# Performance work log

Measured on AMD Instinct MI355X. Metric: run time of the kernel, lower is better.

Reference implementation:

```python
import jax, jax.numpy as jnp
import numpy as np

B, C, H, W = 4, 64, 64, 64

def _conv1x1(x, w, b):
    # Conv2d(k=1): y[b,o,h,w] = sum_c x[b,c,h,w]*w[o,c] + b[o]
    return jnp.einsum('bchw,oc->bohw', x, w) + b[None, :, None, None]

def setup_inputs() -> dict:
    key = jax.random.key(0)
    ks = jax.random.split(key, 8)
    s = 1.0 / np.sqrt(C)
    return {
        'v1': jax.random.normal(ks[0], (B, C, H, W), jnp.float32),
        'v2': jax.random.normal(ks[1], (B, C, H, W), jnp.float32),
        'wq': jax.random.normal(ks[2], (C, C), jnp.float32) * s,
        'bq': jax.random.normal(ks[3], (C,), jnp.float32) * 0.01,
        'wk': jax.random.normal(ks[4], (C, C), jnp.float32) * s,
        'bk': jax.random.normal(ks[5], (C,), jnp.float32) * 0.01,
        'wv': jax.random.normal(ks[6], (C, C), jnp.float32) * s,
        'bv': jax.random.normal(ks[7], (C,), jnp.float32) * 0.01,
    }

def reference(v1, v2, wq, bq, wk, bk, wv, bv):
    q = _conv1x1(v1, wq, bq)   # (B,C,H,W)
    k = _conv1x1(v2, wk, bk)
    v = _conv1x1(v2, wv, bv)
    b, c, h, w = q.shape
    n = c * h                   # tokens = C*H, feature dim = W (matches torch view)
    qf = q.reshape(b, n, w)
    kf = k.reshape(b, n, w)
    vf = v.reshape(b, n, w)
    scores = jnp.einsum('bnw,bmw->bnm', qf, kf)   # (B, N, N)
    attn = jax.nn.softmax(scores, axis=-1)
    out = jnp.einsum('bnm,bmw->bnw', attn, vf)
    return out.reshape(v1.shape)
```

## Files before the change

### kernel.cpp

```cpp
#include <hip/hip_runtime.h>


#define Bn 4
#define Cc 64
#define HW 4096
#define Nn 4096
#define Dd 64
#define TS (Bn * Nn * Dd)
#define LOG2E 1.44269504088896340736f

typedef _Float16 f16;
typedef _Float16 f16x8 __attribute__((ext_vector_type(8)));
typedef _Float16 f16x4 __attribute__((ext_vector_type(4)));
typedef __fp16 fp16x2 __attribute__((ext_vector_type(2)));
typedef float f32x4 __attribute__((ext_vector_type(4)));

__device__ __forceinline__ int swz(int row, int col) {
    return row * 64 + (col ^ ((row & 7) << 3));
}

__device__ __forceinline__ void gl_lds16(const f16* g, f16* l) {
    __builtin_amdgcn_global_load_lds(
        (const __attribute__((address_space(1))) unsigned int*)g,
        (__attribute__((address_space(3))) unsigned int*)l, 16, 0, 0);
}

__global__ __launch_bounds__(256) void qkv_conv(
    const float* __restrict__ v1, const float* __restrict__ v2,
    const float* __restrict__ wq, const float* __restrict__ bq,
    const float* __restrict__ wk, const float* __restrict__ bk,
    const float* __restrict__ wv, const float* __restrict__ bv,
    f16* __restrict__ Qh, f16* __restrict__ Kh, f16* __restrict__ Vh)
{
    const int t    = threadIdx.x;
    const int lane = t & 63;
    const int og   = __builtin_amdgcn_readfirstlane(t >> 6);
    const int b    = blockIdx.y;
    const int p    = blockIdx.x * 64 + lane;
    const int z    = blockIdx.z;
    const int zt   = z >> 1;
    const int ch0  = (z & 1) * 32 + og * 8;

    const float* w    = (zt == 0) ? wq : (zt == 1) ? wk : wv;
    const float* bias = (zt == 0) ? bq : (zt == 1) ? bk : bv;
    const float* x    = ((zt == 0) ? v1 : v2) + (size_t)b * (Cc * HW) + p;

    float acc[8];
    #pragma unroll
    for (int j = 0; j < 8; ++j) acc[j] = bias[ch0 + j];
    #pragma unroll 16
    for (int c = 0; c < 64; ++c) {
        float xc = x[c * HW];
        #pragma unroll
        for (int j = 0; j < 8; ++j)
            acc[j] = fmaf(w[(ch0 + j) * 64 + c], xc, acc[j]);
    }

    f16* dst = (zt == 0) ? Qh : (zt == 1) ? Kh : Vh;
    const float scale = (zt == 0) ? LOG2E : 1.0f;
    #pragma unroll
    for (int j = 0; j < 8; ++j) {
        size_t idx = (size_t)b * (Nn * Dd) + (size_t)(ch0 + j) * 4096 + p;
        dst[idx] = (f16)(acc[j] * scale);
    }
}

__global__ __launch_bounds__(256) void vtrans(const f16* __restrict__ Vh,
                                              f16* __restrict__ Vt)
{
    __shared__ f16 tile[64][72];
    const int t  = threadIdx.x;
    const int n0 = blockIdx.x * 64;
    const int b  = blockIdx.y;
    for (int i = t; i < 4096; i += 256) {
        int r = i >> 6, c = i & 63;
        tile[r][c] = Vh[(size_t)b * (Nn * Dd) + (size_t)(n0 + r) * 64 + c];
    }
    __syncthreads();
    for (int i = t; i < 4096; i += 256) {
        int w = i >> 6, n = i & 63;
        Vt[(size_t)b * (Dd * Nn) + (size_t)w * Nn + n0 + n] = tile[n][w];
    }
}

__global__ __launch_bounds__(512, 4) void attn(
    const f16* __restrict__ Qhg, const f16* __restrict__ Khg,
    const f16* __restrict__ Vtg,
    float* __restrict__ out, f16* __restrict__ Opart, float* __restrict__ lw)
{
    __shared__ __align__(16) f16 KT[2][4096];
    __shared__ __align__(16) f16 VT[2][4096];

    const int t    = threadIdx.x;
    const int lane = t & 63, wvi = t >> 6;
    const int g = lane >> 4, c = lane & 15;
    const int b  = blockIdx.z;
    const int sp = blockIdx.y;
    const int S  = gridDim.y;
    const int n0 = blockIdx.x * 256;
    const int keysPerSplit = Nn / S;
    const int nTiles = keysPerSplit / 64;
    const int kbase = sp * keysPerSplit;

    const int srow = t >> 3;
    const int gc   = ((t & 7) ^ (srow & 7)) * 8;
    f16* ldsKdst0 = &KT[0][(wvi * 8) * 64];
    f16* ldsKdst1 = &KT[1][(wvi * 8) * 64];
    f16* ldsVdst0 = &VT[0][(wvi * 8) * 64];
    f16* ldsVdst1 = &VT[1][(wvi * 8) * 64];

    const f16* Kb = Khg + (size_t)b * (Nn * Dd);
    const f16* Vb = Vtg + (size_t)b * (Dd * Nn);

    f16x8 qbh[2][2];
    #pragma unroll
    for (int qf = 0; qf < 2; ++qf) {
        const int qrow = n0 + wvi * 32 + qf * 16 + c;
        const f16* qhp = Qhg + ((size_t)b * Nn + qrow) * 64;
        #pragma unroll
        for (int ks = 0; ks < 2; ++ks)
            qbh[qf][ks] = *(const f16x8*)(qhp + ks * 32 + g * 8);
    }

    float m_run[2] = {-1e30f, -1e30f}, lpart[2] = {0.f, 0.f};
    f32x4 of[2][4];
    #pragma unroll
    for (int qf = 0; qf < 2; ++qf)
        #pragma unroll
        for (int nf = 0; nf < 4; ++nf)
            #pragma unroll
            for (int r = 0; r < 4; ++r) of[qf][nf][r] = 0.f;

    gl_lds16(Kb + (size_t)(kbase + srow) * 64 + gc, ldsKdst0);
    gl_lds16(Vb + (size_t)srow * Nn + kbase + gc, ldsVdst0);
    __syncthreads();
    int cur = 0;

    for (int kt = 0; kt < nTiles; ++kt) {
        if (kt + 1 < nTiles) {
            const int k0n = kbase + (kt + 1) * 64;
            f16* kd = cur ? ldsKdst0 : ldsKdst1;
            f16* vd = cur ? ldsVdst0 : ldsVdst1;
            gl_lds16(Kb + (size_t)(k0n + srow) * 64 + gc, kd);
            gl_lds16(Vb + (size_t)srow * Nn + k0n + gc, vd);
        }

        const f16* KTc = KT[cur];
        const f16* VTc = VT[cur];

        f32x4 accS[2][4];
        #pragma unroll
        for (int qf = 0; qf < 2; ++qf)
            #pragma unroll
            for (int fm = 0; fm < 4; ++fm)
                #pragma unroll
                for (int r = 0; r < 4; ++r) accS[qf][fm][r] = 0.f;
        #pragma unroll
        for (int fm = 0; fm < 4; ++fm) {
            const int key = fm * 16 + c;
            f16x8 kh0 = *(const f16x8*)(KTc + swz(key, g * 8));
            f16x8 kh1 = *(const f16x8*)(KTc + swz(key, 32 + g * 8));
            #pragma unroll
            for (int qf = 0; qf < 2; ++qf) {
                accS[qf][fm] = __builtin_amdgcn_mfma_f32_16x16x32_f16(kh0, qbh[qf][0], accS[qf][fm], 0, 0, 0);
                accS[qf][fm] = __builtin_amdgcn_mfma_f32_16x16x32_f16(kh1, qbh[qf][1], accS[qf][fm], 0, 0, 0);
            }
        }

        f16x4 pb[2][4];
        #pragma unroll
        for (int qf = 0; qf < 2; ++qf) {
            float m0 = fmaxf(fmaxf(accS[qf][0][0], accS[qf][0][1]),
                             fmaxf(accS[qf][0][2], accS[qf][0][3]));
            float m1 = fmaxf(fmaxf(accS[qf][1][0], accS[qf][1][1]),
                             fmaxf(accS[qf][1][2], accS[qf][1][3]));
            float m2 = fmaxf(fmaxf(accS[qf][2][0], accS[qf][2][1]),
                             fmaxf(accS[qf][2][2], accS[qf][2][3]));
            float m3 = fmaxf(fmaxf(accS[qf][3][0], accS[qf][3][1]),
                             fmaxf(accS[qf][3][2], accS[qf][3][3]));
            float tmax = fmaxf(fmaxf(m0, m1), fmaxf(m2, m3));
            tmax = fmaxf(tmax, __shfl_xor(tmax, 16));
            tmax = fmaxf(tmax, __shfl_xor(tmax, 32));
            if (!__all(tmax <= m_run[qf] + 8.f)) {
                const float mnew = fmaxf(m_run[qf], tmax);
                const float corr = exp2f(m_run[qf] - mnew);
                lpart[qf] *= corr;
                #pragma unroll
                for (int nf = 0; nf < 4; ++nf)
                    #pragma unroll
                    for (int r = 0; r < 4; ++r) of[qf][nf][r] *= corr;
                m_run[qf] = mnew;
            }
            float s01 = 0.f, s23 = 0.f;
            #pragma unroll
            for (int fm = 0; fm < 4; ++fm) {
                #pragma unroll
                for (int r = 0; r < 4; ++r) {
                    float pp = exp2f(accS[qf][fm][r] - m_run[qf]);
                    accS[qf][fm][r] = pp;
                    if (fm < 2) s01 += pp; else s23 += pp;
                }
                union { f16x4 v4; fp16x2 h2[2]; } u;
                u.h2[0] = __builtin_amdgcn_cvt_pkrtz(accS[qf][fm][0], accS[qf][fm][1]);
                u.h2[1] = __builtin_amdgcn_cvt_pkrtz(accS[qf][fm][2], accS[qf][fm][3]);
                pb[qf][fm] = u.v4;
            }
            lpart[qf] += s01 + s23;
        }

        #pragma unroll
        for (int nf = 0; nf < 4; ++nf) {
            #pragma unroll
            for (int fm = 0; fm < 4; ++fm) {
                f16x4 va = *(const f16x4*)(VTc + swz(nf * 16 + c, fm * 16 + g * 4));
                of[0][nf] = __builtin_amdgcn_mfma_f32_16x16x16f16(va, pb[0][fm], of[0][nf], 0, 0, 0);
                of[1][nf] = __builtin_amdgcn_mfma_f32_16x16x16f16(va, pb[1][fm], of[1][nf], 0, 0, 0);
            }
        }

        __syncthreads();
        cur ^= 1;
    }

    if (S == 1) {
        #pragma unroll
        for (int qf = 0; qf < 2; ++qf) {
            float lr = lpart[qf];
            lr += __shfl_xor(lr, 16);
            lr += __shfl_xor(lr, 32);
            const float linv = 1.0f / lr;
            const int n = n0 + wvi * 32 + qf * 16 + c;
            #pragma unroll
            for (int nf = 0; nf < 4; ++nf) {
                float4 o4 = make_float4(of[qf][nf][0] * linv, of[qf][nf][1] * linv,
                                        of[qf][nf][2] * linv, of[qf][nf][3] * linv);
                *(float4*)(out + (((size_t)b * Nn + n) << 6) + nf * 16 + g * 4) = o4;
            }
        }
    } else {
        #pragma unroll
        for (int qf = 0; qf < 2; ++qf) {
            float lr = lpart[qf];
            lr += __shfl_xor(lr, 16);
            lr += __shfl_xor(lr, 32);
            const float linv = 1.0f / lr;
            const int n = n0 + wvi * 32 + qf * 16 + c;
            size_t robase = (((size_t)sp * Bn + b) * Nn + n) << 6;
            #pragma unroll
            for (int nf = 0; nf < 4; ++nf) {
                union { f16x4 v4; fp16x2 h2[2]; } u;
                u.h2[0] = __builtin_amdgcn_cvt_pkrtz(of[qf][nf][0] * linv, of[qf][nf][1] * linv);
                u.h2[1] = __builtin_amdgcn_cvt_pkrtz(of[qf][nf][2] * linv, of[qf][nf][3] * linv);
                *(f16x4*)(Opart + robase + nf * 16 + g * 4) = u.v4;
            }
            if (g == 0) {
                lw[((size_t)sp * Bn + b) * Nn + n] = lr * exp2f(m_run[qf]);
            }
        }
    }
}

__global__ __launch_bounds__(256) void combine(
    const f16* __restrict__ Opart, const float* __restrict__ lw,
    float* __restrict__ out, int S)
{
    const int idx8 = blockIdx.x * 256 + threadIdx.x;
    const int w8 = idx8 & 7;
    const int n  = (idx8 >> 3) & (Nn - 1);
    const int b  = idx8 >> 15;
    float num[8];
    #pragma unroll
    for (int j = 0; j < 8; ++j) num[j] = 0.f;
    float den = 0.f;
    for (int s = 0; s < S; ++s) {
        float a = lw[((size_t)s * Bn + b) * Nn + n];
        f16x8 o8 = *(const f16x8*)(Opart + ((((size_t)s * Bn + b) * Nn + n) << 6) + w8 * 8);
        #pragma unroll
        for (int j = 0; j < 8; ++j) num[j] += a * (float)o8[j];
        den += a;
    }
    const float di = 1.0f / den;
    float* op = out + (((size_t)b * Nn + n) << 6) + w8 * 8;
    float4 lo = make_float4(num[0] * di, num[1] * di, num[2] * di, num[3] * di);
    float4 hi = make_float4(num[4] * di, num[5] * di, num[6] * di, num[7] * di);
    *(float4*)op = lo;
    *(float4*)(op + 4) = hi;
}

extern "C" void kernel_launch(void* const* d_in, const int* in_sizes, int n_in,
                              void* d_out, int out_size, void* d_ws, size_t ws_size,
                              hipStream_t stream)
{
    const float* v1 = (const float*)d_in[0];
    const float* v2 = (const float*)d_in[1];
    const float* wq = (const float*)d_in[2];
    const float* bq = (const float*)d_in[3];
    const float* wk = (const float*)d_in[4];
    const float* bk = (const float*)d_in[5];
    const float* wv = (const float*)d_in[6];
    const float* bv = (const float*)d_in[7];
    float* out = (float*)d_out;

    char* ws = (char*)d_ws;
    const size_t T = (size_t)TS * sizeof(f16);
    f16* Qh = (f16*)(ws + 0 * T);
    f16* Kh = (f16*)(ws + 1 * T);
    f16* Vh = (f16*)(ws + 2 * T);
    f16* Vt = (f16*)(ws + 3 * T);
    const size_t base = 4 * T;
    const size_t opartBytes = (size_t)TS * 2;
    const size_t lwBytes    = (size_t)Bn * Nn * 4;

    int S = 1;
    if      (ws_size >= base + 8 * (opartBytes + lwBytes)) S = 8;
    else if (ws_size >= base + 4 * (opartBytes + lwBytes)) S = 4;
    else if (ws_size >= base + 2 * (opartBytes + lwBytes)) S = 2;

    f16*   Opart = (f16*)(ws + base);
    float* lwp   = (float*)(ws + base + (size_t)S * opartBytes);

    qkv_conv<<<dim3(64, 4, 6), 256, 0, stream>>>(v1, v2, wq, bq, wk, bk, wv, bv,
                                                 Qh, Kh, Vh);
    vtrans<<<dim3(64, 4), 256, 0, stream>>>(Vh, Vt);
    attn<<<dim3(16, S, 4), 512, 0, stream>>>(Qh, Kh, Vt, out, Opart, lwp);
    if (S > 1) {
        combine<<<(Bn * Nn * Dd / 8) / 256, 256, 0, stream>>>(Opart, lwp, out, S);
    }
}
```

Baseline: 69.02 us.

## Compute QKV 1x1 convolutions with MFMA via LDS-staged fp16 tiles

Rewrites the QKV projection kernel to stage weights and a 64x64 input tile in LDS as fp16, then computes the projection with 16x16x32 MFMA instructions instead of scalar FMAs. The grid goes from 6 to 3 z-slices with 512 threads each, so each block covers all 64 output channels and input reads are shared across channels. It adds fp16 rounding of inputs and weights before accumulation, which may change accuracy slightly. The conv is a small part of total time next to attention.

```diff
diff --git a/kernel.cpp b/kernel.cpp
--- a/kernel.cpp
+++ b/kernel.cpp
@@ -25,43 +25,68 @@
         (__attribute__((address_space(3))) unsigned int*)l, 16, 0, 0);
 }
 
-__global__ __launch_bounds__(256) void qkv_conv(
+__global__ __launch_bounds__(512) void qkv_conv(
     const float* __restrict__ v1, const float* __restrict__ v2,
     const float* __restrict__ wq, const float* __restrict__ bq,
     const float* __restrict__ wk, const float* __restrict__ bk,
     const float* __restrict__ wv, const float* __restrict__ bv,
     f16* __restrict__ Qh, f16* __restrict__ Kh, f16* __restrict__ Vh)
 {
+    __shared__ __align__(16) f16 wl[64 * 72];
+    __shared__ __align__(16) f16 Xt[64 * 72];
+    __shared__ __align__(16) float bl[64];
+
     const int t    = threadIdx.x;
-    const int lane = t & 63;
-    const int og   = __builtin_amdgcn_readfirstlane(t >> 6);
-    const int b    = blockIdx.y;
-    const int p    = blockIdx.x * 64 + lane;
-    const int z    = blockIdx.z;
-    const int zt   = z >> 1;
-    const int ch0  = (z & 1) * 32 + og * 8;
-
-    const float* w    = (zt == 0) ? wq : (zt == 1) ? wk : wv;
-    const float* bias = (zt == 0) ? bq : (zt == 1) ? bk : bv;
-    const float* x    = ((zt == 0) ? v1 : v2) + (size_t)b * (Cc * HW) + p;
-
-    float acc[8];
+    const int lane = t & 63, wvi = t >> 6;
+    const int g = lane >> 4, c = lane & 15;
+    const int b   = blockIdx.y;
+    const int blk = blockIdx.x;
+    const int z   = blockIdx.z;
+
+    const float* w    = (z == 0) ? wq : (z == 1) ? wk : wv;
+    const float* bias = (z == 0) ? bq : (z == 1) ? bk : bv;
+    const float* x    = ((z == 0) ? v1 : v2) + (size_t)b * (Cc * HW) + blk * 64;
+    f16* dst          = (z == 0) ? Qh : (z == 1) ? Kh : Vh;
+    const float scale = (z == 0) ? LOG2E : 1.0f;
+
+    for (int i = t; i < 4096; i += 512)
+        wl[(i >> 6) * 72 + (i & 63)] = (f16)(w[i] * scale);
+    if (t < 64) bl[t] = bias[t] * scale;
+    {
+        const int cch = t >> 3, dp0 = (t & 7) * 8;
+        float4 x0 = *(const float4*)(x + (size_t)cch * HW + dp0);
+        float4 x1 = *(const float4*)(x + (size_t)cch * HW + dp0 + 4);
+        Xt[(dp0 + 0) * 72 + cch] = (f16)x0.x;
+        Xt[(dp0 + 1) * 72 + cch] = (f16)x0.y;
+        Xt[(dp0 + 2) * 72 + cch] = (f16)x0.z;
+        Xt[(dp0 + 3) * 72 + cch] = (f16)x0.w;
+        Xt[(dp0 + 4) * 72 + cch] = (f16)x1.x;
+        Xt[(dp0 + 5) * 72 + cch] = (f16)x1.y;
+        Xt[(dp0 + 6) * 72 + cch] = (f16)x1.z;
+        Xt[(dp0 + 7) * 72 + cch] = (f16)x1.w;
+    }
+    __syncthreads();
+
+    const int fn  = wvi & 3;
+    const int fo2 = (wvi >> 2) * 2;
+
+    f16x8 xb0 = *(const f16x8*)(Xt + (fn * 16 + c) * 72 + g * 8);
+    f16x8 xb1 = *(const f16x8*)(Xt + (fn * 16 + c) * 72 + 32 + g * 8);
+
     #pragma unroll
-    for (int j = 0; j < 8; ++j) acc[j] = bias[ch0 + j];
-    #pragma unroll 16
-    for (int c = 0; c < 64; ++c) {
-        float xc = x[c * HW];
-        #pragma unroll
-        for (int j = 0; j < 8; ++j)
-            acc[j] = fmaf(w[(ch0 + j) * 64 + c], xc, acc[j]);
-    }
-
-    f16* dst = (zt == 0) ? Qh : (zt == 1) ? Kh : Vh;
-    const float scale = (zt == 0) ? LOG2E : 1.0f;
-    #pragma unroll
-    for (int j = 0; j < 8; ++j) {
-        size_t idx = (size_t)b * (Nn * Dd) + (size_t)(ch0 + j) * 4096 + p;
-        dst[idx] = (f16)(acc[j] * scale);
+    for (int fi = 0; fi < 2; ++fi) {
+        const int fo = fo2 + fi;
+        f16x8 wa0 = *(const f16x8*)(wl + (fo * 16 + c) * 72 + g * 8);
+        f16x8 wa1 = *(const f16x8*)(wl + (fo * 16 + c) * 72 + 32 + g * 8);
+        f32x4 acc = *(const f32x4*)(bl + fo * 16 + g * 4);
+        acc = __builtin_amdgcn_mfma_f32_16x16x32_f16(wa0, xb0, acc, 0, 0, 0);
+        acc = __builtin_amdgcn_mfma_f32_16x16x32_f16(wa1, xb1, acc, 0, 0, 0);
+        #pragma unroll
+        for (int r = 0; r < 4; ++r) {
+            const int o = fo * 16 + g * 4 + r;
+            const int n = o * 64 + blk;
+            dst[(size_t)b * (Nn * Dd) + (size_t)n * 64 + fn * 16 + c] = (f16)acc[r];
+        }
     }
 }
 
@@ -319,7 +344,7 @@
     f16*   Opart = (f16*)(ws + base);
     float* lwp   = (float*)(ws + base + (size_t)S * opartBytes);
 
-    qkv_conv<<<dim3(64, 4, 6), 256, 0, stream>>>(v1, v2, wq, bq, wk, bk, wv, bv,
+    qkv_conv<<<dim3(64, 4, 3), 512, 0, stream>>>(v1, v2, wq, bq, wk, bk, wv, bv,
                                                  Qh, Kh, Vh);
     vtrans<<<dim3(64, 4), 256, 0, stream>>>(Vh, Vt);
     attn<<<dim3(16, S, 4), 512, 0, stream>>>(Qh, Kh, Vt, out, Opart, lwp);
```

New measurement: 61.24 us. 11.3% less time.
